# Kernel tuning notes

Measured on AMD Instinct MI355X. Metric: run time of the kernel, lower is better.

## Reference

```python
import jax, jax.numpy as jnp
import numpy as np

NUM_HEADS = 8

def setup_inputs() -> dict:
    key = jax.random.key(0)
    k1, k2, k3, k4, k5 = jax.random.split(key, 5)
    B, N, C = 64, 2048, 256
    x = jax.random.normal(k1, (B, N, C), dtype=jnp.float32)
    # weights scaled ~0.02 so softmax logits stay in a sane range
    qkv_w = jax.random.normal(k2, (3 * C, C), dtype=jnp.float32) * 0.02
    qkv_b = jax.random.normal(k3, (3 * C,), dtype=jnp.float32) * 0.02
    proj_w = jax.random.normal(k4, (C, C), dtype=jnp.float32) * 0.02
    proj_b = jax.random.normal(k5, (C,), dtype=jnp.float32) * 0.02
    return {"x": x, "qkv_w": qkv_w, "qkv_b": qkv_b, "proj_w": proj_w, "proj_b": proj_b}

def reference(x, qkv_w, qkv_b, proj_w, proj_b):
    B, N, C = x.shape
    H = NUM_HEADS
    Ch = C // H
    scale = Ch ** (-0.5)
    # qkv: [B,N,3,H,Ch] -- NOTE: original code does NOT permute to (3,B,H,N,Ch),
    # so attention contracts over the channel dim producing [B,N,H,H]
    qkv = (x @ qkv_w.T + qkv_b).reshape(B, N, 3, H, Ch)
    q, k, v = qkv[:, :, 0], qkv[:, :, 1], qkv[:, :, 2]  # each [B,N,H,Ch]
    attn = jnp.einsum('bnhc,bngc->bnhg', q, k) * scale  # [B,N,H,H] attention over heads
    attn = jax.nn.softmax(attn, axis=-1)
    out = jnp.einsum('bnhg,bngc->bnhc', attn, v)        # [B,N,H,Ch]
    # faithful to .transpose(1,2).reshape(B,N,C)
    out = out.transpose(0, 2, 1, 3).reshape(B, N, C)
    return out @ proj_w.T + proj_b
```

## Files before the change

### kernel.cpp

```cpp
#include <hip/hip_runtime.h>
#include <hip/hip_bf16.h>


typedef __attribute__((ext_vector_type(8))) short bf16x8;
typedef __attribute__((ext_vector_type(4))) short bf16x4;
typedef __attribute__((ext_vector_type(4))) float f32x4;

__device__ __forceinline__ short f2bf(float f) {
    unsigned u = __builtin_bit_cast(unsigned, f);
    unsigned r = (u + 0x7FFFu + ((u >> 16) & 1u)) >> 16;
    return (short)r;
}
__device__ __forceinline__ float bf2f(short h) {
    unsigned u = ((unsigned)(unsigned short)h) << 16;
    return __builtin_bit_cast(float, u);
}

__global__ void k0_convert(const float* __restrict__ qkv_w,
                           const float* __restrict__ proj_w,
                           short* __restrict__ wq_bf,
                           short* __restrict__ wp_bf) {
    int i = blockIdx.x * 256 + threadIdx.x;
    if (i < 196608) {
        wq_bf[i] = f2bf(qkv_w[i]);
    } else {
        int j = i - 196608;
        wp_bf[j] = f2bf(proj_w[j]);
    }
}

__global__ __launch_bounds__(512, 4) void k1_qkv_attn(
    const float* __restrict__ x,
    const short* __restrict__ wq,
    const float* __restrict__ qkv_b,
    short* __restrict__ out2)
{
    __shared__ __align__(16) char smem[49664];
    const int tid  = threadIdx.x;
    const int lane = tid & 63;
    const int wave = tid >> 6;
    const long t0  = (long)blockIdx.x * 32;

    {
        const int r = tid >> 4, s = tid & 15;
        const float4* src = (const float4*)(x + (t0 + r) * 256 + s * 16);
        float ff[16];
        float4 f0 = src[0], f1 = src[1], f2 = src[2], f3 = src[3];
        ff[0]=f0.x; ff[1]=f0.y; ff[2]=f0.z; ff[3]=f0.w;
        ff[4]=f1.x; ff[5]=f1.y; ff[6]=f1.z; ff[7]=f1.w;
        ff[8]=f2.x; ff[9]=f2.y; ff[10]=f2.z; ff[11]=f2.w;
        ff[12]=f3.x; ff[13]=f3.y; ff[14]=f3.z; ff[15]=f3.w;
        bf16x8 v0, v1;
#pragma unroll
        for (int i = 0; i < 8; ++i) { v0[i] = f2bf(ff[i]); v1[i] = f2bf(ff[8 + i]); }
        const int swz = (r & 7) << 4;
        *(bf16x8*)(smem + r * 512 + ((s * 32) ^ swz))      = v0;
        *(bf16x8*)(smem + r * 512 + ((s * 32 + 16) ^ swz)) = v1;
    }
    __syncthreads();

    f32x4 acc[2][6];
#pragma unroll
    for (int i = 0; i < 2; ++i)
#pragma unroll
        for (int j = 0; j < 6; ++j) acc[i][j] = (f32x4){0.f, 0.f, 0.f, 0.f};

    const int fr = lane & 15, fq = lane >> 4;
    const int nb = wave * 96;
    const short* wq_base = wq + (nb + fr) * 256 + fq * 8;

#pragma unroll
    for (int ks = 0; ks < 8; ++ks) {
        bf16x8 aW[6], bX[2];
#pragma unroll
        for (int j = 0; j < 6; ++j)
            aW[j] = *(const bf16x8*)(wq_base + j * 16 * 256 + ks * 32);
        const int kbyte = (ks * 32 + fq * 8) * 2;
#pragma unroll
        for (int i = 0; i < 2; ++i) {
            const int row = i * 16 + fr;
            bX[i] = *(const bf16x8*)(smem + row * 512 + (kbyte ^ ((row & 7) << 4)));
        }
#pragma unroll
        for (int i = 0; i < 2; ++i)
#pragma unroll
            for (int j = 0; j < 6; ++j)
                acc[i][j] = __builtin_amdgcn_mfma_f32_16x16x32_bf16(aW[j], bX[i], acc[i][j], 0, 0, 0);
    }
    __syncthreads();

#pragma unroll
    for (int i = 0; i < 2; ++i) {
        const int tok = i * 16 + fr;
#pragma unroll
        for (int j = 0; j < 6; ++j) {
            const int n0 = nb + j * 16 + fq * 4;
            float4 bias = *(const float4*)(qkv_b + n0);
            float bb[4] = {bias.x, bias.y, bias.z, bias.w};
            bf16x4 y;
#pragma unroll
            for (int r = 0; r < 4; ++r) y[r] = f2bf(acc[i][j][r] + bb[r]);
            *(bf16x4*)(smem + tok * 1552 + n0 * 2) = y;
        }
    }
    __syncthreads();

    {
        const int t = tid >> 4, sub = tid & 15;
        const int h = sub & 7, half = sub >> 3;
        const char* Yrow = smem + t * 1552;
        const float scale = 0.17677669529663687f;

        float q[16];
        {
            bf16x8 q0 = *(const bf16x8*)(Yrow + (h * 32 + half * 16) * 2);
            bf16x8 q1 = *(const bf16x8*)(Yrow + (h * 32 + half * 16 + 8) * 2);
#pragma unroll
            for (int c = 0; c < 8; ++c) { q[c] = bf2f(q0[c]); q[8 + c] = bf2f(q1[c]); }
        }
        float s[8];
#pragma unroll
        for (int g = 0; g < 8; ++g) {
            bf16x8 k0 = *(const bf16x8*)(Yrow + (256 + g * 32 + half * 16) * 2);
            bf16x8 k1 = *(const bf16x8*)(Yrow + (256 + g * 32 + half * 16 + 8) * 2);
            float p = 0.f;
#pragma unroll
            for (int c = 0; c < 8; ++c) { p += q[c] * bf2f(k0[c]); p += q[8 + c] * bf2f(k1[c]); }
            p += __shfl_xor(p, 8);
            s[g] = p * scale;
        }
        float mx = s[0];
#pragma unroll
        for (int g = 1; g < 8; ++g) mx = fmaxf(mx, s[g]);
        float pw[8], psum = 0.f;
#pragma unroll
        for (int g = 0; g < 8; ++g) { pw[g] = __expf(s[g] - mx); psum += pw[g]; }
        const float inv = 1.f / psum;

        float o[16];
#pragma unroll
        for (int c = 0; c < 16; ++c) o[c] = 0.f;
#pragma unroll
        for (int g = 0; g < 8; ++g) {
            bf16x8 v0 = *(const bf16x8*)(Yrow + (512 + g * 32 + half * 16) * 2);
            bf16x8 v1 = *(const bf16x8*)(Yrow + (512 + g * 32 + half * 16 + 8) * 2);
#pragma unroll
            for (int c = 0; c < 8; ++c) { o[c] += pw[g] * bf2f(v0[c]); o[8 + c] += pw[g] * bf2f(v1[c]); }
        }

        const long tg = t0 + t;
        const long b  = tg >> 11;
        const int  n  = (int)(tg & 2047);
        const int  np = (h * 2048 + n) >> 3;
        const int  cp = (n & 7) * 32 + half * 16;
        short* dst = out2 + ((b * 2048 + np) * 256 + cp);
        bf16x8 o0, o1;
#pragma unroll
        for (int c = 0; c < 8; ++c) { o0[c] = f2bf(o[c] * inv); o1[c] = f2bf(o[8 + c] * inv); }
        *(bf16x8*)(dst)     = o0;
        *(bf16x8*)(dst + 8) = o1;
    }
}

__global__ __launch_bounds__(512, 4) void k2_proj(
    const short* __restrict__ out2,
    const short* __restrict__ wp,
    const float* __restrict__ proj_b,
    float* __restrict__ out)
{
    __shared__ __align__(16) char smem[64 * 512];
    const int tid  = threadIdx.x;
    const int lane = tid & 63;
    const int wave = tid >> 6;
    const long t0  = (long)blockIdx.x * 64;

    {
        const int r = tid >> 3, sgm = tid & 7;
        const char* src = (const char*)out2 + (t0 + r) * 512 + sgm * 64;
        const int swz = (r & 7) << 4;
#pragma unroll
        for (int u = 0; u < 4; ++u) {
            bf16x8 v = *(const bf16x8*)(src + u * 16);
            const int off = sgm * 64 + u * 16;
            *(bf16x8*)(smem + r * 512 + (off ^ swz)) = v;
        }
    }
    __syncthreads();

    f32x4 acc[4][2];
#pragma unroll
    for (int i = 0; i < 4; ++i)
#pragma unroll
        for (int j = 0; j < 2; ++j) acc[i][j] = (f32x4){0.f, 0.f, 0.f, 0.f};

    const int fr = lane & 15, fq = lane >> 4;
    const int nb = wave * 32;
    const short* wp_base = wp + (nb + fr) * 256 + fq * 8;

#pragma unroll
    for (int ks = 0; ks < 8; ++ks) {
        bf16x8 aW[2], bX[4];
#pragma unroll
        for (int j = 0; j < 2; ++j)
            aW[j] = *(const bf16x8*)(wp_base + j * 16 * 256 + ks * 32);
        const int kbyte = (ks * 32 + fq * 8) * 2;
#pragma unroll
        for (int i = 0; i < 4; ++i) {
            const int row = i * 16 + fr;
            bX[i] = *(const bf16x8*)(smem + row * 512 + (kbyte ^ ((row & 7) << 4)));
        }
#pragma unroll
        for (int i = 0; i < 4; ++i)
#pragma unroll
            for (int j = 0; j < 2; ++j)
                acc[i][j] = __builtin_amdgcn_mfma_f32_16x16x32_bf16(aW[j], bX[i], acc[i][j], 0, 0, 0);
    }

#pragma unroll
    for (int i = 0; i < 4; ++i) {
        const long tok = t0 + i * 16 + fr;
#pragma unroll
        for (int j = 0; j < 2; ++j) {
            const int n0 = nb + j * 16 + fq * 4;
            float4 bias = *(const float4*)(proj_b + n0);
            float4 res;
            res.x = acc[i][j][0] + bias.x;
            res.y = acc[i][j][1] + bias.y;
            res.z = acc[i][j][2] + bias.z;
            res.w = acc[i][j][3] + bias.w;
            *(float4*)(out + tok * 256 + n0) = res;
        }
    }
}

extern "C" void kernel_launch(void* const* d_in, const int* in_sizes, int n_in,
                              void* d_out, int out_size, void* d_ws, size_t ws_size,
                              hipStream_t stream) {
    const float* x      = (const float*)d_in[0];
    const float* qkv_w  = (const float*)d_in[1];
    const float* qkv_b  = (const float*)d_in[2];
    const float* proj_w = (const float*)d_in[3];
    const float* proj_b = (const float*)d_in[4];
    float* out = (float*)d_out;

    char* ws = (char*)d_ws;
    short* out2  = (short*)ws;
    short* wq_bf = (short*)(ws + 67108864);
    short* wp_bf = (short*)(ws + 67108864 + 393216);

    k0_convert<<<1024, 256, 0, stream>>>(qkv_w, proj_w, wq_bf, wp_bf);
    k1_qkv_attn<<<4096, 512, 0, stream>>>(x, wq_bf, qkv_b, out2);
    k2_proj<<<2048, 512, 0, stream>>>(out2, wp_bf, proj_b, out);
}
```

Measured before the change: 453.3 us.

## Fuse QKV, head attention and output projection into one kernel

Merges the attention kernel and the projection kernel into a single kernel working on 16-token blocks. The transpose-reshape maps each 16-token block onto 16 output rows, so the attention result is staged in shared memory and projected in place. This removes the 64 MB bf16 intermediate round trip through global memory and one kernel launch. In exchange the weight matrices are re-read by twice as many blocks, each wave now issues fewer MFMAs per weight load, and the kernel has extra barriers.

```diff
diff --git a/kernel.cpp b/kernel.cpp
--- a/kernel.cpp
+++ b/kernel.cpp
@@ -24,211 +24,167 @@
     if (i < 196608) {
         wq_bf[i] = f2bf(qkv_w[i]);
     } else {
-        int j = i - 196608;
-        wp_bf[j] = f2bf(proj_w[j]);
-    }
-}
-
-__global__ __launch_bounds__(512, 4) void k1_qkv_attn(
+        wp_bf[i - 196608] = f2bf(proj_w[i - 196608]);
+    }
+}
+
+__global__ __launch_bounds__(512, 6) void k1_fused(
     const float* __restrict__ x,
     const short* __restrict__ wq,
     const float* __restrict__ qkv_b,
-    short* __restrict__ out2)
-{
-    __shared__ __align__(16) char smem[49664];
-    const int tid  = threadIdx.x;
-    const int lane = tid & 63;
-    const int wave = tid >> 6;
-    const long t0  = (long)blockIdx.x * 32;
-
-    {
-        const int r = tid >> 4, s = tid & 15;
-        const float4* src = (const float4*)(x + (t0 + r) * 256 + s * 16);
-        float ff[16];
-        float4 f0 = src[0], f1 = src[1], f2 = src[2], f3 = src[3];
-        ff[0]=f0.x; ff[1]=f0.y; ff[2]=f0.z; ff[3]=f0.w;
-        ff[4]=f1.x; ff[5]=f1.y; ff[6]=f1.z; ff[7]=f1.w;
-        ff[8]=f2.x; ff[9]=f2.y; ff[10]=f2.z; ff[11]=f2.w;
-        ff[12]=f3.x; ff[13]=f3.y; ff[14]=f3.z; ff[15]=f3.w;
-        bf16x8 v0, v1;
-#pragma unroll
-        for (int i = 0; i < 8; ++i) { v0[i] = f2bf(ff[i]); v1[i] = f2bf(ff[8 + i]); }
-        const int swz = (r & 7) << 4;
-        *(bf16x8*)(smem + r * 512 + ((s * 32) ^ swz))      = v0;
-        *(bf16x8*)(smem + r * 512 + ((s * 32 + 16) ^ swz)) = v1;
-    }
-    __syncthreads();
-
-    f32x4 acc[2][6];
-#pragma unroll
-    for (int i = 0; i < 2; ++i)
-#pragma unroll
-        for (int j = 0; j < 6; ++j) acc[i][j] = (f32x4){0.f, 0.f, 0.f, 0.f};
-
-    const int fr = lane & 15, fq = lane >> 4;
-    const int nb = wave * 96;
-    const short* wq_base = wq + (nb + fr) * 256 + fq * 8;
-
-#pragma unroll
-    for (int ks = 0; ks < 8; ++ks) {
-        bf16x8 aW[6], bX[2];
-#pragma unroll
-        for (int j = 0; j < 6; ++j)
-            aW[j] = *(const bf16x8*)(wq_base + j * 16 * 256 + ks * 32);
-        const int kbyte = (ks * 32 + fq * 8) * 2;
-#pragma unroll
-        for (int i = 0; i < 2; ++i) {
-            const int row = i * 16 + fr;
-            bX[i] = *(const bf16x8*)(smem + row * 512 + (kbyte ^ ((row & 7) << 4)));
-        }
-#pragma unroll
-        for (int i = 0; i < 2; ++i)
-#pragma unroll
-            for (int j = 0; j < 6; ++j)
-                acc[i][j] = __builtin_amdgcn_mfma_f32_16x16x32_bf16(aW[j], bX[i], acc[i][j], 0, 0, 0);
-    }
-    __syncthreads();
-
-#pragma unroll
-    for (int i = 0; i < 2; ++i) {
-        const int tok = i * 16 + fr;
-#pragma unroll
-        for (int j = 0; j < 6; ++j) {
-            const int n0 = nb + j * 16 + fq * 4;
-            float4 bias = *(const float4*)(qkv_b + n0);
-            float bb[4] = {bias.x, bias.y, bias.z, bias.w};
-            bf16x4 y;
-#pragma unroll
-            for (int r = 0; r < 4; ++r) y[r] = f2bf(acc[i][j][r] + bb[r]);
-            *(bf16x4*)(smem + tok * 1552 + n0 * 2) = y;
-        }
-    }
-    __syncthreads();
-
-    {
-        const int t = tid >> 4, sub = tid & 15;
-        const int h = sub & 7, half = sub >> 3;
-        const char* Yrow = smem + t * 1552;
-        const float scale = 0.17677669529663687f;
-
-        float q[16];
-        {
-            bf16x8 q0 = *(const bf16x8*)(Yrow + (h * 32 + half * 16) * 2);
-            bf16x8 q1 = *(const bf16x8*)(Yrow + (h * 32 + half * 16 + 8) * 2);
-#pragma unroll
-            for (int c = 0; c < 8; ++c) { q[c] = bf2f(q0[c]); q[8 + c] = bf2f(q1[c]); }
-        }
-        float s[8];
-#pragma unroll
-        for (int g = 0; g < 8; ++g) {
-            bf16x8 k0 = *(const bf16x8*)(Yrow + (256 + g * 32 + half * 16) * 2);
-            bf16x8 k1 = *(const bf16x8*)(Yrow + (256 + g * 32 + half * 16 + 8) * 2);
-            float p = 0.f;
-#pragma unroll
-            for (int c = 0; c < 8; ++c) { p += q[c] * bf2f(k0[c]); p += q[8 + c] * bf2f(k1[c]); }
-            p += __shfl_xor(p, 8);
-            s[g] = p * scale;
-        }
-        float mx = s[0];
-#pragma unroll
-        for (int g = 1; g < 8; ++g) mx = fmaxf(mx, s[g]);
-        float pw[8], psum = 0.f;
-#pragma unroll
-        for (int g = 0; g < 8; ++g) { pw[g] = __expf(s[g] - mx); psum += pw[g]; }
-        const float inv = 1.f / psum;
-
-        float o[16];
-#pragma unroll
-        for (int c = 0; c < 16; ++c) o[c] = 0.f;
-#pragma unroll
-        for (int g = 0; g < 8; ++g) {
-            bf16x8 v0 = *(const bf16x8*)(Yrow + (512 + g * 32 + half * 16) * 2);
-            bf16x8 v1 = *(const bf16x8*)(Yrow + (512 + g * 32 + half * 16 + 8) * 2);
-#pragma unroll
-            for (int c = 0; c < 8; ++c) { o[c] += pw[g] * bf2f(v0[c]); o[8 + c] += pw[g] * bf2f(v1[c]); }
-        }
-
-        const long tg = t0 + t;
-        const long b  = tg >> 11;
-        const int  n  = (int)(tg & 2047);
-        const int  np = (h * 2048 + n) >> 3;
-        const int  cp = (n & 7) * 32 + half * 16;
-        short* dst = out2 + ((b * 2048 + np) * 256 + cp);
-        bf16x8 o0, o1;
-#pragma unroll
-        for (int c = 0; c < 8; ++c) { o0[c] = f2bf(o[c] * inv); o1[c] = f2bf(o[8 + c] * inv); }
-        *(bf16x8*)(dst)     = o0;
-        *(bf16x8*)(dst + 8) = o1;
-    }
-}
-
-__global__ __launch_bounds__(512, 4) void k2_proj(
-    const short* __restrict__ out2,
     const short* __restrict__ wp,
     const float* __restrict__ proj_b,
     float* __restrict__ out)
 {
-    __shared__ __align__(16) char smem[64 * 512];
+    __shared__ __align__(16) char smem[24832];
     const int tid  = threadIdx.x;
     const int lane = tid & 63;
     const int wave = tid >> 6;
-    const long t0  = (long)blockIdx.x * 64;
-
-    {
-        const int r = tid >> 3, sgm = tid & 7;
-        const char* src = (const char*)out2 + (t0 + r) * 512 + sgm * 64;
-        const int swz = (r & 7) << 4;
-#pragma unroll
-        for (int u = 0; u < 4; ++u) {
-            bf16x8 v = *(const bf16x8*)(src + u * 16);
-            const int off = sgm * 64 + u * 16;
-            *(bf16x8*)(smem + r * 512 + (off ^ swz)) = v;
-        }
-    }
-    __syncthreads();
-
-    f32x4 acc[4][2];
-#pragma unroll
-    for (int i = 0; i < 4; ++i)
-#pragma unroll
-        for (int j = 0; j < 2; ++j) acc[i][j] = (f32x4){0.f, 0.f, 0.f, 0.f};
+    const int t0   = blockIdx.x * 16;
 
     const int fr = lane & 15, fq = lane >> 4;
-    const int nb = wave * 32;
-    const short* wp_base = wp + (nb + fr) * 256 + fq * 8;
-
-#pragma unroll
-    for (int ks = 0; ks < 8; ++ks) {
-        bf16x8 aW[2], bX[4];
-#pragma unroll
-        for (int j = 0; j < 2; ++j)
-            aW[j] = *(const bf16x8*)(wp_base + j * 16 * 256 + ks * 32);
-        const int kbyte = (ks * 32 + fq * 8) * 2;
-#pragma unroll
-        for (int i = 0; i < 4; ++i) {
-            const int row = i * 16 + fr;
-            bX[i] = *(const bf16x8*)(smem + row * 512 + (kbyte ^ ((row & 7) << 4)));
-        }
-#pragma unroll
-        for (int i = 0; i < 4; ++i)
-#pragma unroll
-            for (int j = 0; j < 2; ++j)
-                acc[i][j] = __builtin_amdgcn_mfma_f32_16x16x32_bf16(aW[j], bX[i], acc[i][j], 0, 0, 0);
-    }
-
-#pragma unroll
-    for (int i = 0; i < 4; ++i) {
-        const long tok = t0 + i * 16 + fr;
-#pragma unroll
-        for (int j = 0; j < 2; ++j) {
-            const int n0 = nb + j * 16 + fq * 4;
+
+    {
+        const int r = tid >> 5, s = tid & 31;
+        const float4* src = (const float4*)(x + (long)(t0 + r) * 256 + s * 8);
+        float4 f0 = src[0], f1 = src[1];
+        bf16x8 v;
+        v[0] = f2bf(f0.x); v[1] = f2bf(f0.y); v[2] = f2bf(f0.z); v[3] = f2bf(f0.w);
+        v[4] = f2bf(f1.x); v[5] = f2bf(f1.y); v[6] = f2bf(f1.z); v[7] = f2bf(f1.w);
+        *(bf16x8*)(smem + r * 512 + ((s * 16) ^ ((r & 7) << 4))) = v;
+    }
+    __syncthreads();
+
+    f32x4 acc[6];
+#pragma unroll
+    for (int j = 0; j < 6; ++j) acc[j] = (f32x4){0.f, 0.f, 0.f, 0.f};
+    {
+        const int nbq = wave * 96;
+        const short* wq_base = wq + (nbq + fr) * 256 + fq * 8;
+#pragma unroll
+        for (int ks = 0; ks < 8; ++ks) {
+            const int kbyte = ks * 64 + fq * 16;
+            bf16x8 bX = *(const bf16x8*)(smem + fr * 512 + (kbyte ^ ((fr & 7) << 4)));
+            bf16x8 aW0 = *(const bf16x8*)(wq_base + 0 * 4096 + ks * 32);
+            bf16x8 aW1 = *(const bf16x8*)(wq_base + 1 * 4096 + ks * 32);
+            bf16x8 aW2 = *(const bf16x8*)(wq_base + 2 * 4096 + ks * 32);
+            acc[0] = __builtin_amdgcn_mfma_f32_16x16x32_bf16(aW0, bX, acc[0], 0, 0, 0);
+            acc[1] = __builtin_amdgcn_mfma_f32_16x16x32_bf16(aW1, bX, acc[1], 0, 0, 0);
+            acc[2] = __builtin_amdgcn_mfma_f32_16x16x32_bf16(aW2, bX, acc[2], 0, 0, 0);
+            bf16x8 aW3 = *(const bf16x8*)(wq_base + 3 * 4096 + ks * 32);
+            bf16x8 aW4 = *(const bf16x8*)(wq_base + 4 * 4096 + ks * 32);
+            bf16x8 aW5 = *(const bf16x8*)(wq_base + 5 * 4096 + ks * 32);
+            acc[3] = __builtin_amdgcn_mfma_f32_16x16x32_bf16(aW3, bX, acc[3], 0, 0, 0);
+            acc[4] = __builtin_amdgcn_mfma_f32_16x16x32_bf16(aW4, bX, acc[4], 0, 0, 0);
+            acc[5] = __builtin_amdgcn_mfma_f32_16x16x32_bf16(aW5, bX, acc[5], 0, 0, 0);
+        }
+    }
+    __syncthreads();
+
+    {
+        const int nbq = wave * 96;
+#pragma unroll
+        for (int j = 0; j < 6; ++j) {
+            const int n0 = nbq + j * 16 + fq * 4;
+            float4 bias = *(const float4*)(qkv_b + n0);
+            bf16x4 y;
+            y[0] = f2bf(acc[j][0] + bias.x);
+            y[1] = f2bf(acc[j][1] + bias.y);
+            y[2] = f2bf(acc[j][2] + bias.z);
+            y[3] = f2bf(acc[j][3] + bias.w);
+            *(bf16x4*)(smem + fr * 1552 + n0 * 2) = y;
+        }
+    }
+    __syncthreads();
+
+    float o[8];
+    int orow, ocol;
+    {
+        const int t = tid >> 5, sub = tid & 31;
+        const int h = sub & 7, qt = sub >> 3;
+        const char* Yrow = smem + t * 1552;
+        const float scale = 0.17677669529663687f;
+
+        float q[8];
+        {
+            bf16x8 qv = *(const bf16x8*)(Yrow + h * 64 + qt * 16);
+#pragma unroll
+            for (int c = 0; c < 8; ++c) q[c] = bf2f(qv[c]);
+        }
+        float s[8];
+#pragma unroll
+        for (int g = 0; g < 8; ++g) {
+            bf16x8 kv = *(const bf16x8*)(Yrow + 512 + g * 64 + qt * 16);
+            float p = 0.f;
+#pragma unroll
+            for (int c = 0; c < 8; ++c) p += q[c] * bf2f(kv[c]);
+            p += __shfl_xor(p, 8);
+            p += __shfl_xor(p, 16);
+            s[g] = p * scale;
+        }
+        float mx = s[0];
+#pragma unroll
+        for (int g = 1; g < 8; ++g) mx = fmaxf(mx, s[g]);
+        float pw[8], psum = 0.f;
+#pragma unroll
+        for (int g = 0; g < 8; ++g) { pw[g] = __expf(s[g] - mx); psum += pw[g]; }
+        const float inv = 1.f / psum;
+
+#pragma unroll
+        for (int c = 0; c < 8; ++c) o[c] = 0.f;
+#pragma unroll
+        for (int g = 0; g < 8; ++g) {
+            bf16x8 vv = *(const bf16x8*)(Yrow + 1024 + g * 64 + qt * 16);
+#pragma unroll
+            for (int c = 0; c < 8; ++c) o[c] += pw[g] * bf2f(vv[c]);
+        }
+#pragma unroll
+        for (int c = 0; c < 8; ++c) o[c] *= inv;
+
+        orow = h * 2 + (t >> 3);
+        ocol = (t & 7) * 64 + qt * 16;
+    }
+    __syncthreads();
+
+    {
+        bf16x8 ov;
+#pragma unroll
+        for (int c = 0; c < 8; ++c) ov[c] = f2bf(o[c]);
+        *(bf16x8*)(smem + orow * 512 + (ocol ^ ((orow & 7) << 4))) = ov;
+    }
+    __syncthreads();
+
+    {
+        const int nbp = wave * 32;
+        const short* wp_base = wp + (nbp + fr) * 256 + fq * 8;
+        f32x4 pacc0 = (f32x4){0.f, 0.f, 0.f, 0.f};
+        f32x4 pacc1 = (f32x4){0.f, 0.f, 0.f, 0.f};
+#pragma unroll
+        for (int ks = 0; ks < 8; ++ks) {
+            bf16x8 bO = *(const bf16x8*)(smem + fr * 512 + ((ks * 64 + fq * 16) ^ ((fr & 7) << 4)));
+            bf16x8 w0 = *(const bf16x8*)(wp_base + ks * 32);
+            bf16x8 w1 = *(const bf16x8*)(wp_base + 4096 + ks * 32);
+            pacc0 = __builtin_amdgcn_mfma_f32_16x16x32_bf16(w0, bO, pacc0, 0, 0, 0);
+            pacc1 = __builtin_amdgcn_mfma_f32_16x16x32_bf16(w1, bO, pacc1, 0, 0, 0);
+        }
+
+        const int  h   = fr >> 1, oct = fr & 1;
+        const long b   = (long)(t0 >> 11);
+        const int  n   = t0 & 2047;
+        const long rp  = b * 2048 + h * 256 + (n >> 3) + oct;
+        {
+            const int n0 = nbp + fq * 4;
             float4 bias = *(const float4*)(proj_b + n0);
-            float4 res;
-            res.x = acc[i][j][0] + bias.x;
-            res.y = acc[i][j][1] + bias.y;
-            res.z = acc[i][j][2] + bias.z;
-            res.w = acc[i][j][3] + bias.w;
-            *(float4*)(out + tok * 256 + n0) = res;
+            float4 res = {pacc0[0] + bias.x, pacc0[1] + bias.y,
+                          pacc0[2] + bias.z, pacc0[3] + bias.w};
+            *(float4*)(out + rp * 256 + n0) = res;
+        }
+        {
+            const int n0 = nbp + 16 + fq * 4;
+            float4 bias = *(const float4*)(proj_b + n0);
+            float4 res = {pacc1[0] + bias.x, pacc1[1] + bias.y,
+                          pacc1[2] + bias.z, pacc1[3] + bias.w};
+            *(float4*)(out + rp * 256 + n0) = res;
         }
     }
 }
@@ -244,11 +200,9 @@
     float* out = (float*)d_out;
 
     char* ws = (char*)d_ws;
-    short* out2  = (short*)ws;
-    short* wq_bf = (short*)(ws + 67108864);
-    short* wp_bf = (short*)(ws + 67108864 + 393216);
+    short* wq_bf = (short*)ws;
+    short* wp_bf = (short*)(ws + 393216);
 
     k0_convert<<<1024, 256, 0, stream>>>(qkv_w, proj_w, wq_bf, wp_bf);
-    k1_qkv_attn<<<4096, 512, 0, stream>>>(x, wq_bf, qkv_b, out2);
-    k2_proj<<<2048, 512, 0, stream>>>(out2, wp_bf, proj_b, out);
-}
+    k1_fused<<<8192, 512, 0, stream>>>(x, wq_bf, qkv_b, wp_bf, proj_b, out);
+}
```

After: 658.3 us. 1.45x slower.
